# Kernel tuning notes

Measured on AMD Instinct MI355X. Metric: run time of the kernel, lower is better.

## Reference

```python
import jax, jax.numpy as jnp
import numpy as np

N_NODES = 100000


def sage_conv(x, src, dst, w_self, w_neigh, b):
    # DGL SAGEConv('mean'): h = x @ W_self + mean_{u in N(v)} x_u @ W_neigh + b
    ones = jnp.ones(src.shape[0], dtype=x.dtype)
    deg = jax.ops.segment_sum(ones, dst, num_segments=N_NODES)  # [N]
    neigh_sum = jax.ops.segment_sum(x[src], dst, num_segments=N_NODES)  # [N, F]
    neigh = neigh_sum / jnp.clip(deg, 1.0)[:, None]  # isolated nodes -> 0
    return x @ w_self + neigh @ w_neigh + b


def setup_inputs() -> dict:
    key = jax.random.key(0)
    ks = jax.random.split(key, 9)
    nfeat, nhid, nclass = 128, 128, 2
    E = 1600000
    x = jax.random.normal(ks[0], (N_NODES, nfeat), dtype=jnp.float32)
    src = jax.random.randint(ks[1], (E,), 0, N_NODES)
    dst = jax.random.randint(ks[2], (E,), 0, N_NODES)
    s1 = 1.0 / np.sqrt(nfeat)
    s2 = 1.0 / np.sqrt(nhid)
    return {
        "x": x,
        "src": src,
        "dst": dst,
        "w_self1": jax.random.uniform(ks[3], (nfeat, nhid), jnp.float32, -s1, s1),
        "w_neigh1": jax.random.uniform(ks[4], (nfeat, nhid), jnp.float32, -s1, s1),
        "b1": jnp.zeros((nhid,), jnp.float32),
        "w_self2": jax.random.uniform(ks[5], (nhid, nclass), jnp.float32, -s2, s2),
        "w_neigh2": jax.random.uniform(ks[6], (nhid, nclass), jnp.float32, -s2, s2),
        "b2": jnp.zeros((nclass,), jnp.float32),
    }


def reference(x, src, dst, w_self1, w_neigh1, b1, w_self2, w_neigh2, b2):
    h = jax.nn.relu(sage_conv(x, src, dst, w_self1, w_neigh1, b1))
    h = sage_conv(h, src, dst, w_self2, w_neigh2, b2)
    return jax.nn.log_softmax(h, axis=1)
```

## Files before the change

kernel.cpp:

```cpp
#include <hip/hip_runtime.h>
#include <hip/hip_bf16.h>


#define N_FEAT 128
#define CSHIFT 10
#define CNODES 1024
#define CCAP 18432
#define BATCH 4096
#define BF_BLOCKS 256
#define PW_BLOCKS 128

typedef __attribute__((ext_vector_type(8))) short short8;
typedef __attribute__((ext_vector_type(8))) unsigned short ushort8_t;
typedef __attribute__((ext_vector_type(16))) float f32x16;

__global__ __launch_bounds__(256) void prep_and_split_kernel(
    const int* __restrict__ src, const int* __restrict__ dst,
    int* __restrict__ ccursor, unsigned* __restrict__ cbuf, int E,
    const float* __restrict__ x, ushort* __restrict__ xb, int n4,
    const float* __restrict__ w1, const float* __restrict__ w2,
    ushort* __restrict__ wt, int nms) {
    __shared__ unsigned stage[BATCH];
    __shared__ int cntw[4][128];
    __shared__ int curw[4][128];
    __shared__ int s[128];
    __shared__ int excl[128];
    __shared__ int incl[128];
    __shared__ int gpos[128];
    int tid = threadIdx.x;
    int bid = blockIdx.x;

    if (bid >= nms) {
        int rb = bid - nms;
        if (rb < BF_BLOCKS) {
            int i = rb * 256 + tid;
            int stride = BF_BLOCKS * 256;
            for (; i < n4; i += stride) {
                float4 v = ((const float4*)x)[i];
                ushort4 r;
                r.x = __bfloat16_as_ushort(__float2bfloat16(v.x));
                r.y = __bfloat16_as_ushort(__float2bfloat16(v.y));
                r.z = __bfloat16_as_ushort(__float2bfloat16(v.z));
                r.w = __bfloat16_as_ushort(__float2bfloat16(v.w));
                ((ushort4*)xb)[i] = r;
            }
        } else {
            int id = (rb - BF_BLOCKS) * 256 + tid;
            int nn = id >> 8;
            int k = id & 255;
            float v = (k < 128) ? w1[k * 128 + nn] : w2[(k - 128) * 128 + nn];
            wt[nn * 256 + k] = __bfloat16_as_ushort(__float2bfloat16(v));
        }
        return;
    }

    int wv = tid >> 6;
    int base = bid * BATCH;
    int total = min(BATCH, E - base);

    unsigned pk[16];
    int bn[16];
    for (int i = tid; i < 512; i += 256) ((int*)cntw)[i] = 0;
    __syncthreads();
    #pragma unroll
    for (int k = 0; k < 16; ++k) {
        int e = base + k * 256 + tid;
        if (e < E) {
            int d = dst[e];
            int sv = src[e];
            bn[k] = d >> CSHIFT;
            pk[k] = ((unsigned)(d & (CNODES - 1)) << 17) | (unsigned)sv;
            atomicAdd(&cntw[wv][bn[k]], 1);
        } else {
            bn[k] = -1;
        }
    }
    __syncthreads();
    int c = 0;
    if (tid < 128) {
        int c0 = cntw[0][tid], c1 = cntw[1][tid], c2 = cntw[2][tid], c3 = cntw[3][tid];
        cntw[0][tid] = 0;
        cntw[1][tid] = c0;
        cntw[2][tid] = c0 + c1;
        cntw[3][tid] = c0 + c1 + c2;
        c = c0 + c1 + c2 + c3;
        s[tid] = c;
    }
    __syncthreads();
    int val = c;
    for (int off = 1; off < 128; off <<= 1) {
        int t = (tid >= off && tid < 128) ? s[tid - off] : 0;
        __syncthreads();
        if (tid < 128) { val += t; s[tid] = val; }
        __syncthreads();
    }
    if (tid < 128) {
        incl[tid] = val;
        int e0 = val - c;
        excl[tid] = e0;
        curw[0][tid] = e0 + cntw[0][tid];
        curw[1][tid] = e0 + cntw[1][tid];
        curw[2][tid] = e0 + cntw[2][tid];
        curw[3][tid] = e0 + cntw[3][tid];
        gpos[tid] = (c > 0) ? atomicAdd(&ccursor[tid], c) : 0;
    }
    __syncthreads();
    #pragma unroll
    for (int k = 0; k < 16; ++k) {
        if (bn[k] >= 0) {
            int ofs = atomicAdd(&curw[wv][bn[k]], 1);
            stage[ofs] = pk[k];
        }
    }
    __syncthreads();
    for (int i = tid; i < total; i += 256) {
        int lo = 0, hi = 127;
        while (lo < hi) {
            int mid = (lo + hi) >> 1;
            if (incl[mid] > i) hi = mid; else lo = mid + 1;
        }
        int b = lo;
        int target = gpos[b] + (i - excl[b]);
        cbuf[(size_t)b * CCAP + target] = stage[i];
    }
}

__global__ __launch_bounds__(1024) void build_csr2_kernel(
    const unsigned* __restrict__ cbuf, const int* __restrict__ ccnt,
    int* __restrict__ row_ptr, int* __restrict__ csr, int N, int E) {
    __shared__ int hist[CNODES];
    __shared__ int s[CNODES];
    __shared__ int cur[CNODES];
    __shared__ int cstart_s;
    int cb = blockIdx.x;
    int tid = threadIdx.x;

    int c0 = 0;
    if (tid < 128) { c0 = ccnt[tid]; s[tid] = c0; }
    __syncthreads();
    int v128 = c0;
    for (int off = 1; off < 128; off <<= 1) {
        int t = (tid >= off && tid < 128) ? s[tid - off] : 0;
        __syncthreads();
        if (tid < 128) { v128 += t; s[tid] = v128; }
        __syncthreads();
    }
    if (tid == cb) cstart_s = v128 - c0;
    if (cb == 0 && tid == 0) row_ptr[N] = E;
    __syncthreads();
    int cnt = ccnt[cb];
    int base = cstart_s;
    size_t bbase = (size_t)cb * CCAP;

    hist[tid] = 0;
    __syncthreads();
    for (int e = tid; e < cnt; e += 1024) {
        unsigned p = cbuf[bbase + e];
        atomicAdd(&hist[p >> 17], 1);
    }
    __syncthreads();
    int c = hist[tid];
    int val = c;
    s[tid] = val;
    __syncthreads();
    for (int off = 1; off < 1024; off <<= 1) {
        int t = (tid >= off) ? s[tid - off] : 0;
        __syncthreads();
        val += t;
        s[tid] = val;
        __syncthreads();
    }
    int excl = val - c;
    int node = cb * CNODES + tid;
    if (node < N) row_ptr[node] = base + excl;
    cur[tid] = excl;
    __syncthreads();
    for (int e = tid; e < cnt; e += 1024) {
        unsigned p = cbuf[bbase + e];
        int bin = p >> 17;
        int ofs = atomicAdd(&cur[bin], 1);
        csr[base + ofs] = (int)(p & 0x1FFFF);
    }
}

__device__ __forceinline__ float bf16_bits_to_f32(ushort u) {
    union { unsigned int i; float f; } c;
    c.i = ((unsigned int)u) << 16;
    return c.f;
}

__global__ void aggregate_bf16_kernel(const ushort* __restrict__ xb,
                                      const int* __restrict__ row_ptr,
                                      const int* __restrict__ csr,
                                      ushort* __restrict__ out, int n) {
    int v = blockIdx.x * 4 + (threadIdx.x >> 6);
    int lane = threadIdx.x & 63;
    if (v >= n) return;
    int beg = row_ptr[v];
    int end = row_ptr[v + 1];
    float a0 = 0.f, b0 = 0.f, a1 = 0.f, b1 = 0.f;
    int e = beg;
    for (; e + 8 <= end; e += 8) {
        int s0 = csr[e],     s1 = csr[e + 1], s2 = csr[e + 2], s3 = csr[e + 3];
        int s4 = csr[e + 4], s5 = csr[e + 5], s6 = csr[e + 6], s7 = csr[e + 7];
        ushort2 t0 = ((const ushort2*)(xb + (size_t)s0 * N_FEAT))[lane];
        ushort2 t1 = ((const ushort2*)(xb + (size_t)s1 * N_FEAT))[lane];
        ushort2 t2 = ((const ushort2*)(xb + (size_t)s2 * N_FEAT))[lane];
        ushort2 t3 = ((const ushort2*)(xb + (size_t)s3 * N_FEAT))[lane];
        ushort2 t4 = ((const ushort2*)(xb + (size_t)s4 * N_FEAT))[lane];
        ushort2 t5 = ((const ushort2*)(xb + (size_t)s5 * N_FEAT))[lane];
        ushort2 t6 = ((const ushort2*)(xb + (size_t)s6 * N_FEAT))[lane];
        ushort2 t7 = ((const ushort2*)(xb + (size_t)s7 * N_FEAT))[lane];
        a0 += bf16_bits_to_f32(t0.x); b0 += bf16_bits_to_f32(t0.y);
        a1 += bf16_bits_to_f32(t1.x); b1 += bf16_bits_to_f32(t1.y);
        a0 += bf16_bits_to_f32(t2.x); b0 += bf16_bits_to_f32(t2.y);
        a1 += bf16_bits_to_f32(t3.x); b1 += bf16_bits_to_f32(t3.y);
        a0 += bf16_bits_to_f32(t4.x); b0 += bf16_bits_to_f32(t4.y);
        a1 += bf16_bits_to_f32(t5.x); b1 += bf16_bits_to_f32(t5.y);
        a0 += bf16_bits_to_f32(t6.x); b0 += bf16_bits_to_f32(t6.y);
        a1 += bf16_bits_to_f32(t7.x); b1 += bf16_bits_to_f32(t7.y);
    }
    for (; e + 4 <= end; e += 4) {
        int s0 = csr[e], s1 = csr[e + 1], s2 = csr[e + 2], s3 = csr[e + 3];
        ushort2 t0 = ((const ushort2*)(xb + (size_t)s0 * N_FEAT))[lane];
        ushort2 t1 = ((const ushort2*)(xb + (size_t)s1 * N_FEAT))[lane];
        ushort2 t2 = ((const ushort2*)(xb + (size_t)s2 * N_FEAT))[lane];
        ushort2 t3 = ((const ushort2*)(xb + (size_t)s3 * N_FEAT))[lane];
        a0 += bf16_bits_to_f32(t0.x); b0 += bf16_bits_to_f32(t0.y);
        a1 += bf16_bits_to_f32(t1.x); b1 += bf16_bits_to_f32(t1.y);
        a0 += bf16_bits_to_f32(t2.x); b0 += bf16_bits_to_f32(t2.y);
        a1 += bf16_bits_to_f32(t3.x); b1 += bf16_bits_to_f32(t3.y);
    }
    for (; e < end; ++e) {
        int s0 = csr[e];
        ushort2 t0 = ((const ushort2*)(xb + (size_t)s0 * N_FEAT))[lane];
        a0 += bf16_bits_to_f32(t0.x); b0 += bf16_bits_to_f32(t0.y);
    }
    int deg = end - beg;
    float inv = (deg > 0) ? 1.0f / (float)deg : 0.0f;
    ushort2 r;
    r.x = __bfloat16_as_ushort(__float2bfloat16((a0 + a1) * inv));
    r.y = __bfloat16_as_ushort(__float2bfloat16((b0 + b1) * inv));
    ((ushort2*)(out + (size_t)v * N_FEAT))[lane] = r;
}

__global__ __launch_bounds__(256) void gemm1_fused_kernel(
    const ushort* __restrict__ xb, const ushort* __restrict__ nbb,
    const ushort* __restrict__ wt, const float* __restrict__ b,
    const float* __restrict__ ws2, const float* __restrict__ wn2,
    float* __restrict__ s_out, float* __restrict__ z_out, int n) {
    __shared__ ushort As[128 * 72];
    __shared__ ushort Bs[128 * 72];
    int tid = threadIdx.x;
    int wave = tid >> 6;
    int lane = tid & 63;
    int m = lane & 31;
    int half = lane >> 5;
    int block_row = blockIdx.x * 128;

    f32x16 acc[4];
    #pragma unroll
    for (int t = 0; t < 4; ++t)
        #pragma unroll
        for (int i = 0; i < 16; ++i) acc[t][i] = 0.0f;

    for (int kc = 0; kc < 4; ++kc) {
        const ushort* A = (kc < 2) ? xb : nbb;
        int k0 = (kc & 1) * 64;
        #pragma unroll
        for (int l = 0; l < 4; ++l) {
            int idx = l * 256 + tid;
            int r = idx >> 3;
            int p = idx & 7;
            int node = block_row + r;
            ushort8_t v;
            if (node < n) {
                v = *(const ushort8_t*)(A + (size_t)node * N_FEAT + k0 + p * 8);
            } else {
                #pragma unroll
                for (int q = 0; q < 8; ++q) v[q] = 0;
            }
            *(ushort8_t*)(&As[r * 72 + p * 8]) = v;
        }
        #pragma unroll
        for (int l = 0; l < 4; ++l) {
            int idx = l * 256 + tid;
            int cc = idx >> 3;
            int p = idx & 7;
            ushort8_t v = *(const ushort8_t*)(wt + (size_t)cc * 256 + kc * 64 + p * 8);
            *(ushort8_t*)(&Bs[cc * 72 + p * 8]) = v;
        }
        __syncthreads();
        #pragma unroll
        for (int ks = 0; ks < 4; ++ks) {
            int koff = ks * 16 + half * 8;
            short8 a = *(const short8*)(&As[(32 * wave + m) * 72 + koff]);
            short8 bf0 = *(const short8*)(&Bs[(0 * 32 + m) * 72 + koff]);
            short8 bf1 = *(const short8*)(&Bs[(1 * 32 + m) * 72 + koff]);
            short8 bf2 = *(const short8*)(&Bs[(2 * 32 + m) * 72 + koff]);
            short8 bf3 = *(const short8*)(&Bs[(3 * 32 + m) * 72 + koff]);
            acc[0] = __builtin_amdgcn_mfma_f32_32x32x16_bf16(a, bf0, acc[0], 0, 0, 0);
            acc[1] = __builtin_amdgcn_mfma_f32_32x32x16_bf16(a, bf1, acc[1], 0, 0, 0);
            acc[2] = __builtin_amdgcn_mfma_f32_32x32x16_bf16(a, bf2, acc[2], 0, 0, 0);
            acc[3] = __builtin_amdgcn_mfma_f32_32x32x16_bf16(a, bf3, acc[3], 0, 0, 0);
        }
        __syncthreads();
    }

    float bcol[4], wsc[4][2], wnc[4][2];
    #pragma unroll
    for (int t = 0; t < 4; ++t) {
        int col = t * 32 + m;
        bcol[t] = b[col];
        float2 a = ((const float2*)ws2)[col];
        float2 q = ((const float2*)wn2)[col];
        wsc[t][0] = a.x; wsc[t][1] = a.y;
        wnc[t][0] = q.x; wnc[t][1] = q.y;
    }
    #pragma unroll
    for (int reg = 0; reg < 16; ++reg) {
        int rowin = (reg & 3) + 8 * (reg >> 2) + 4 * half;
        int node = block_row + 32 * wave + rowin;
        float p0 = 0.f, p1 = 0.f, q0 = 0.f, q1 = 0.f;
        #pragma unroll
        for (int t = 0; t < 4; ++t) {
            float hv = fmaxf(acc[t][reg] + bcol[t], 0.0f);
            p0 += hv * wsc[t][0]; p1 += hv * wsc[t][1];
            q0 += hv * wnc[t][0]; q1 += hv * wnc[t][1];
        }
        #pragma unroll
        for (int off = 1; off < 32; off <<= 1) {
            p0 += __shfl_xor(p0, off);
            p1 += __shfl_xor(p1, off);
            q0 += __shfl_xor(q0, off);
            q1 += __shfl_xor(q1, off);
        }
        if (m == 0 && node < n) {
            ((float2*)s_out)[node] = make_float2(p0, p1);
            ((float2*)z_out)[node] = make_float2(q0, q1);
        }
    }
}

__global__ void layer2b_kernel(const float* __restrict__ s_in, const float* __restrict__ z,
                               const int* __restrict__ row_ptr, const int* __restrict__ csr,
                               const float* __restrict__ b, float* __restrict__ out, int n) {
    int v = blockIdx.x * 256 + threadIdx.x;
    if (v >= n) return;
    int beg = row_ptr[v];
    int end = row_ptr[v + 1];
    float a0 = 0.f, a1 = 0.f, c0 = 0.f, c1 = 0.f;
    int e = beg;
    for (; e + 2 <= end; e += 2) {
        float2 t0 = ((const float2*)z)[csr[e]];
        float2 t1 = ((const float2*)z)[csr[e + 1]];
        a0 += t0.x; a1 += t0.y;
        c0 += t1.x; c1 += t1.y;
    }
    if (e < end) {
        float2 t0 = ((const float2*)z)[csr[e]];
        a0 += t0.x; a1 += t0.y;
    }
    int deg = end - beg;
    float inv = (deg > 0) ? 1.0f / (float)deg : 0.0f;
    float2 sv = ((const float2*)s_in)[v];
    float o0 = sv.x + (a0 + c0) * inv + b[0];
    float o1 = sv.y + (a1 + c1) * inv + b[1];
    float mx = fmaxf(o0, o1);
    float lse = mx + logf(expf(o0 - mx) + expf(o1 - mx));
    ((float2*)out)[v] = make_float2(o0 - lse, o1 - lse);
}

extern "C" void kernel_launch(void* const* d_in, const int* in_sizes, int n_in,
                              void* d_out, int out_size, void* d_ws, size_t ws_size,
                              hipStream_t stream) {
    const float* x        = (const float*)d_in[0];
    const int*   src      = (const int*)d_in[1];
    const int*   dst      = (const int*)d_in[2];
    const float* w_self1  = (const float*)d_in[3];
    const float* w_neigh1 = (const float*)d_in[4];
    const float* b1       = (const float*)d_in[5];
    const float* w_self2  = (const float*)d_in[6];
    const float* w_neigh2 = (const float*)d_in[7];
    const float* b2       = (const float*)d_in[8];
    float* out = (float*)d_out;

    int N = in_sizes[0] / N_FEAT;
    int E = in_sizes[1];
    int nbk = (N + CNODES - 1) / CNODES;
    int nms = (E + BATCH - 1) / BATCH;

    char* ws = (char*)d_ws;
    size_t off = 0;
    auto alloc = [&](size_t bytes) -> void* {
        void* p = ws + off;
        off += (bytes + 255) & ~(size_t)255;
        return p;
    };
    int*      ccursor = (int*)alloc(128 * 4);
    int*      row_ptr = (int*)alloc((size_t)(N + 1) * 4);
    int*      csr     = (int*)alloc((size_t)E * 4);
    unsigned* cbuf    = (unsigned*)alloc((size_t)nbk * CCAP * 4);
    ushort*   xb      = (ushort*)alloc((size_t)N * N_FEAT * 2);
    ushort*   nbb     = (ushort*)alloc((size_t)N * N_FEAT * 2);
    ushort*   wt      = (ushort*)alloc((size_t)128 * 256 * 2);
    float*    s_buf   = (float*)alloc((size_t)N * 2 * 4);
    float*    z_buf   = (float*)alloc((size_t)N * 2 * 4);
    (void)ws_size; (void)n_in; (void)out_size;

    hipMemsetAsync(ccursor, 0, 128 * 4, stream);

    prep_and_split_kernel<<<nms + BF_BLOCKS + PW_BLOCKS, 256, 0, stream>>>(
        src, dst, ccursor, cbuf, E, x, xb, N * N_FEAT / 4, w_self1, w_neigh1, wt, nms);
    build_csr2_kernel<<<nbk, 1024, 0, stream>>>(cbuf, ccursor, row_ptr, csr, N, E);
    aggregate_bf16_kernel<<<(N + 3) / 4, 256, 0, stream>>>(xb, row_ptr, csr, nbb, N);
    gemm1_fused_kernel<<<(N + 127) / 128, 256, 0, stream>>>(
        xb, nbb, wt, b1, w_self2, w_neigh2, s_buf, z_buf, N);
    layer2b_kernel<<<(N + 255) / 256, 256, 0, stream>>>(s_buf, z_buf, row_ptr, csr, b2, out, N);
}
```

Before: 250.3 us.

## Use 16-byte gathers in aggregation and shuffle-based scans with 512-node CSR buckets

The aggregation kernel now splits each wave into four 16-lane groups. Each lane loads 8 bf16 features (16 bytes) per neighbor, so four neighbors are gathered in parallel, and the partial sums are combined with cross-lane shuffles. The bucket split moves to 256 bins of 512 nodes, which raises the number of CSR build blocks and lowers their size. The LDS-based prefix scans in both the split and build kernels become wave shuffle scans, cutting barrier counts. In exchange, the shuffle reductions add work and the bucket capacity per bin is tighter.

```diff
diff --git a/kernel.cpp b/kernel.cpp
--- a/kernel.cpp
+++ b/kernel.cpp
@@ -3,9 +3,10 @@
 
 
 #define N_FEAT 128
-#define CSHIFT 10
-#define CNODES 1024
-#define CCAP 18432
+#define CSHIFT 9
+#define CNODES 512
+#define NBINS 256
+#define CCAP 9728
 #define BATCH 4096
 #define BF_BLOCKS 256
 #define PW_BLOCKS 128
@@ -13,6 +14,12 @@
 typedef __attribute__((ext_vector_type(8))) short short8;
 typedef __attribute__((ext_vector_type(8))) unsigned short ushort8_t;
 typedef __attribute__((ext_vector_type(16))) float f32x16;
+
+__device__ __forceinline__ float bf16_bits_to_f32(ushort u) {
+    union { unsigned int i; float f; } c;
+    c.i = ((unsigned int)u) << 16;
+    return c.f;
+}
 
 __global__ __launch_bounds__(256) void prep_and_split_kernel(
     const int* __restrict__ src, const int* __restrict__ dst,
@@ -21,12 +28,12 @@
     const float* __restrict__ w1, const float* __restrict__ w2,
     ushort* __restrict__ wt, int nms) {
     __shared__ unsigned stage[BATCH];
-    __shared__ int cntw[4][128];
-    __shared__ int curw[4][128];
-    __shared__ int s[128];
-    __shared__ int excl[128];
-    __shared__ int incl[128];
-    __shared__ int gpos[128];
+    __shared__ int cntw[4][NBINS];
+    __shared__ int curw[4][NBINS];
+    __shared__ int excl[NBINS];
+    __shared__ int incl[NBINS];
+    __shared__ int gpos[NBINS];
+    __shared__ int wsum[4];
     int tid = threadIdx.x;
     int bid = blockIdx.x;
 
@@ -55,12 +62,13 @@
     }
 
     int wv = tid >> 6;
+    int lane = tid & 63;
     int base = bid * BATCH;
     int total = min(BATCH, E - base);
 
     unsigned pk[16];
     int bn[16];
-    for (int i = tid; i < 512; i += 256) ((int*)cntw)[i] = 0;
+    for (int i = tid; i < 4 * NBINS; i += 256) ((int*)cntw)[i] = 0;
     __syncthreads();
     #pragma unroll
     for (int k = 0; k < 16; ++k) {
@@ -76,34 +84,31 @@
         }
     }
     __syncthreads();
-    int c = 0;
-    if (tid < 128) {
-        int c0 = cntw[0][tid], c1 = cntw[1][tid], c2 = cntw[2][tid], c3 = cntw[3][tid];
-        cntw[0][tid] = 0;
-        cntw[1][tid] = c0;
-        cntw[2][tid] = c0 + c1;
-        cntw[3][tid] = c0 + c1 + c2;
-        c = c0 + c1 + c2 + c3;
-        s[tid] = c;
-    }
-    __syncthreads();
+    int c0 = cntw[0][tid], c1 = cntw[1][tid], c2 = cntw[2][tid], c3 = cntw[3][tid];
+    cntw[0][tid] = 0;
+    cntw[1][tid] = c0;
+    cntw[2][tid] = c0 + c1;
+    cntw[3][tid] = c0 + c1 + c2;
+    int c = c0 + c1 + c2 + c3;
     int val = c;
-    for (int off = 1; off < 128; off <<= 1) {
-        int t = (tid >= off && tid < 128) ? s[tid - off] : 0;
-        __syncthreads();
-        if (tid < 128) { val += t; s[tid] = val; }
-        __syncthreads();
-    }
-    if (tid < 128) {
-        incl[tid] = val;
-        int e0 = val - c;
-        excl[tid] = e0;
-        curw[0][tid] = e0 + cntw[0][tid];
-        curw[1][tid] = e0 + cntw[1][tid];
-        curw[2][tid] = e0 + cntw[2][tid];
-        curw[3][tid] = e0 + cntw[3][tid];
-        gpos[tid] = (c > 0) ? atomicAdd(&ccursor[tid], c) : 0;
-    }
+    #pragma unroll
+    for (int off = 1; off < 64; off <<= 1) {
+        int t = __shfl_up(val, off);
+        if (lane >= off) val += t;
+    }
+    if (lane == 63) wsum[wv] = val;
+    __syncthreads();
+    #pragma unroll
+    for (int i = 0; i < 4; ++i)
+        if (i < wv) val += wsum[i];
+    incl[tid] = val;
+    int e0 = val - c;
+    excl[tid] = e0;
+    curw[0][tid] = e0 + cntw[0][tid];
+    curw[1][tid] = e0 + cntw[1][tid];
+    curw[2][tid] = e0 + cntw[2][tid];
+    curw[3][tid] = e0 + cntw[3][tid];
+    gpos[tid] = (c > 0) ? atomicAdd(&ccursor[tid], c) : 0;
     __syncthreads();
     #pragma unroll
     for (int k = 0; k < 16; ++k) {
@@ -114,7 +119,7 @@
     }
     __syncthreads();
     for (int i = tid; i < total; i += 256) {
-        int lo = 0, hi = 127;
+        int lo = 0, hi = NBINS - 1;
         while (lo < hi) {
             int mid = (lo + hi) >> 1;
             if (incl[mid] > i) hi = mid; else lo = mid + 1;
@@ -125,57 +130,59 @@
     }
 }
 
-__global__ __launch_bounds__(1024) void build_csr2_kernel(
+__global__ __launch_bounds__(512) void build_csr2_kernel(
     const unsigned* __restrict__ cbuf, const int* __restrict__ ccnt,
     int* __restrict__ row_ptr, int* __restrict__ csr, int N, int E) {
     __shared__ int hist[CNODES];
-    __shared__ int s[CNODES];
     __shared__ int cur[CNODES];
+    __shared__ int wred[8];
     __shared__ int cstart_s;
     int cb = blockIdx.x;
     int tid = threadIdx.x;
-
-    int c0 = 0;
-    if (tid < 128) { c0 = ccnt[tid]; s[tid] = c0; }
-    __syncthreads();
-    int v128 = c0;
-    for (int off = 1; off < 128; off <<= 1) {
-        int t = (tid >= off && tid < 128) ? s[tid - off] : 0;
-        __syncthreads();
-        if (tid < 128) { v128 += t; s[tid] = v128; }
-        __syncthreads();
-    }
-    if (tid == cb) cstart_s = v128 - c0;
+    int lane = tid & 63;
+    int w = tid >> 6;
+
+    int v = (tid < cb) ? ccnt[tid] : 0;
+    #pragma unroll
+    for (int off = 32; off > 0; off >>= 1) v += __shfl_xor(v, off);
+    if (lane == 0) wred[w] = v;
+    hist[tid] = 0;
+    __syncthreads();
+    if (tid == 0) {
+        int t = 0;
+        #pragma unroll
+        for (int i = 0; i < 8; ++i) t += wred[i];
+        cstart_s = t;
+    }
     if (cb == 0 && tid == 0) row_ptr[N] = E;
-    __syncthreads();
     int cnt = ccnt[cb];
+    size_t bbase = (size_t)cb * CCAP;
+    __syncthreads();
     int base = cstart_s;
-    size_t bbase = (size_t)cb * CCAP;
-
-    hist[tid] = 0;
-    __syncthreads();
-    for (int e = tid; e < cnt; e += 1024) {
+
+    for (int e = tid; e < cnt; e += 512) {
         unsigned p = cbuf[bbase + e];
         atomicAdd(&hist[p >> 17], 1);
     }
     __syncthreads();
     int c = hist[tid];
     int val = c;
-    s[tid] = val;
-    __syncthreads();
-    for (int off = 1; off < 1024; off <<= 1) {
-        int t = (tid >= off) ? s[tid - off] : 0;
-        __syncthreads();
-        val += t;
-        s[tid] = val;
-        __syncthreads();
-    }
+    #pragma unroll
+    for (int off = 1; off < 64; off <<= 1) {
+        int t = __shfl_up(val, off);
+        if (lane >= off) val += t;
+    }
+    if (lane == 63) wred[w] = val;
+    __syncthreads();
+    #pragma unroll
+    for (int i = 0; i < 8; ++i)
+        if (i < w) val += wred[i];
     int excl = val - c;
     int node = cb * CNODES + tid;
     if (node < N) row_ptr[node] = base + excl;
     cur[tid] = excl;
     __syncthreads();
-    for (int e = tid; e < cnt; e += 1024) {
+    for (int e = tid; e < cnt; e += 512) {
         unsigned p = cbuf[bbase + e];
         int bin = p >> 17;
         int ofs = atomicAdd(&cur[bin], 1);
@@ -183,65 +190,78 @@
     }
 }
 
-__device__ __forceinline__ float bf16_bits_to_f32(ushort u) {
-    union { unsigned int i; float f; } c;
-    c.i = ((unsigned int)u) << 16;
-    return c.f;
-}
-
-__global__ void aggregate_bf16_kernel(const ushort* __restrict__ xb,
-                                      const int* __restrict__ row_ptr,
-                                      const int* __restrict__ csr,
-                                      ushort* __restrict__ out, int n) {
+__global__ __launch_bounds__(256) void aggregate_bf16_kernel(
+    const ushort* __restrict__ xb, const int* __restrict__ row_ptr,
+    const int* __restrict__ csr, ushort* __restrict__ out, int n) {
     int v = blockIdx.x * 4 + (threadIdx.x >> 6);
     int lane = threadIdx.x & 63;
+    int sub = lane >> 4;
+    int fc = lane & 15;
     if (v >= n) return;
     int beg = row_ptr[v];
     int end = row_ptr[v + 1];
-    float a0 = 0.f, b0 = 0.f, a1 = 0.f, b1 = 0.f;
+    float acc[8];
+    #pragma unroll
+    for (int j = 0; j < 8; ++j) acc[j] = 0.f;
+    const ushort* xfc = xb + fc * 8;
     int e = beg;
-    for (; e + 8 <= end; e += 8) {
-        int s0 = csr[e],     s1 = csr[e + 1], s2 = csr[e + 2], s3 = csr[e + 3];
-        int s4 = csr[e + 4], s5 = csr[e + 5], s6 = csr[e + 6], s7 = csr[e + 7];
-        ushort2 t0 = ((const ushort2*)(xb + (size_t)s0 * N_FEAT))[lane];
-        ushort2 t1 = ((const ushort2*)(xb + (size_t)s1 * N_FEAT))[lane];
-        ushort2 t2 = ((const ushort2*)(xb + (size_t)s2 * N_FEAT))[lane];
-        ushort2 t3 = ((const ushort2*)(xb + (size_t)s3 * N_FEAT))[lane];
-        ushort2 t4 = ((const ushort2*)(xb + (size_t)s4 * N_FEAT))[lane];
-        ushort2 t5 = ((const ushort2*)(xb + (size_t)s5 * N_FEAT))[lane];
-        ushort2 t6 = ((const ushort2*)(xb + (size_t)s6 * N_FEAT))[lane];
-        ushort2 t7 = ((const ushort2*)(xb + (size_t)s7 * N_FEAT))[lane];
-        a0 += bf16_bits_to_f32(t0.x); b0 += bf16_bits_to_f32(t0.y);
-        a1 += bf16_bits_to_f32(t1.x); b1 += bf16_bits_to_f32(t1.y);
-        a0 += bf16_bits_to_f32(t2.x); b0 += bf16_bits_to_f32(t2.y);
-        a1 += bf16_bits_to_f32(t3.x); b1 += bf16_bits_to_f32(t3.y);
-        a0 += bf16_bits_to_f32(t4.x); b0 += bf16_bits_to_f32(t4.y);
-        a1 += bf16_bits_to_f32(t5.x); b1 += bf16_bits_to_f32(t5.y);
-        a0 += bf16_bits_to_f32(t6.x); b0 += bf16_bits_to_f32(t6.y);
-        a1 += bf16_bits_to_f32(t7.x); b1 += bf16_bits_to_f32(t7.y);
-    }
-    for (; e + 4 <= end; e += 4) {
-        int s0 = csr[e], s1 = csr[e + 1], s2 = csr[e + 2], s3 = csr[e + 3];
-        ushort2 t0 = ((const ushort2*)(xb + (size_t)s0 * N_FEAT))[lane];
-        ushort2 t1 = ((const ushort2*)(xb + (size_t)s1 * N_FEAT))[lane];
-        ushort2 t2 = ((const ushort2*)(xb + (size_t)s2 * N_FEAT))[lane];
-        ushort2 t3 = ((const ushort2*)(xb + (size_t)s3 * N_FEAT))[lane];
-        a0 += bf16_bits_to_f32(t0.x); b0 += bf16_bits_to_f32(t0.y);
-        a1 += bf16_bits_to_f32(t1.x); b1 += bf16_bits_to_f32(t1.y);
-        a0 += bf16_bits_to_f32(t2.x); b0 += bf16_bits_to_f32(t2.y);
-        a1 += bf16_bits_to_f32(t3.x); b1 += bf16_bits_to_f32(t3.y);
-    }
-    for (; e < end; ++e) {
-        int s0 = csr[e];
-        ushort2 t0 = ((const ushort2*)(xb + (size_t)s0 * N_FEAT))[lane];
-        a0 += bf16_bits_to_f32(t0.x); b0 += bf16_bits_to_f32(t0.y);
-    }
-    int deg = end - beg;
-    float inv = (deg > 0) ? 1.0f / (float)deg : 0.0f;
-    ushort2 r;
-    r.x = __bfloat16_as_ushort(__float2bfloat16((a0 + a1) * inv));
-    r.y = __bfloat16_as_ushort(__float2bfloat16((b0 + b1) * inv));
-    ((ushort2*)(out + (size_t)v * N_FEAT))[lane] = r;
+    for (; e + 16 <= end; e += 16) {
+        int s0 = csr[e + sub];
+        int s1 = csr[e + 4 + sub];
+        int s2 = csr[e + 8 + sub];
+        int s3 = csr[e + 12 + sub];
+        ushort8_t t0 = *(const ushort8_t*)(xfc + (size_t)s0 * N_FEAT);
+        ushort8_t t1 = *(const ushort8_t*)(xfc + (size_t)s1 * N_FEAT);
+        ushort8_t t2 = *(const ushort8_t*)(xfc + (size_t)s2 * N_FEAT);
+        ushort8_t t3 = *(const ushort8_t*)(xfc + (size_t)s3 * N_FEAT);
+        #pragma unroll
+        for (int j = 0; j < 8; ++j) acc[j] += bf16_bits_to_f32(t0[j]);
+        #pragma unroll
+        for (int j = 0; j < 8; ++j) acc[j] += bf16_bits_to_f32(t1[j]);
+        #pragma unroll
+        for (int j = 0; j < 8; ++j) acc[j] += bf16_bits_to_f32(t2[j]);
+        #pragma unroll
+        for (int j = 0; j < 8; ++j) acc[j] += bf16_bits_to_f32(t3[j]);
+    }
+    if (e + 8 <= end) {
+        int s0 = csr[e + sub];
+        int s1 = csr[e + 4 + sub];
+        ushort8_t t0 = *(const ushort8_t*)(xfc + (size_t)s0 * N_FEAT);
+        ushort8_t t1 = *(const ushort8_t*)(xfc + (size_t)s1 * N_FEAT);
+        #pragma unroll
+        for (int j = 0; j < 8; ++j) acc[j] += bf16_bits_to_f32(t0[j]);
+        #pragma unroll
+        for (int j = 0; j < 8; ++j) acc[j] += bf16_bits_to_f32(t1[j]);
+        e += 8;
+    }
+    if (e + 4 <= end) {
+        int s0 = csr[e + sub];
+        ushort8_t t0 = *(const ushort8_t*)(xfc + (size_t)s0 * N_FEAT);
+        #pragma unroll
+        for (int j = 0; j < 8; ++j) acc[j] += bf16_bits_to_f32(t0[j]);
+        e += 4;
+    }
+    int rem = end - e;
+    if (sub < rem) {
+        int s0 = csr[e + sub];
+        ushort8_t t0 = *(const ushort8_t*)(xfc + (size_t)s0 * N_FEAT);
+        #pragma unroll
+        for (int j = 0; j < 8; ++j) acc[j] += bf16_bits_to_f32(t0[j]);
+    }
+    #pragma unroll
+    for (int j = 0; j < 8; ++j) {
+        acc[j] += __shfl_xor(acc[j], 16);
+        acc[j] += __shfl_xor(acc[j], 32);
+    }
+    if (lane < 16) {
+        int deg = end - beg;
+        float inv = (deg > 0) ? 1.0f / (float)deg : 0.0f;
+        ushort8_t r;
+        #pragma unroll
+        for (int j = 0; j < 8; ++j)
+            r[j] = __bfloat16_as_ushort(__float2bfloat16(acc[j] * inv));
+        *(ushort8_t*)(out + (size_t)v * N_FEAT + lane * 8) = r;
+    }
 }
 
 __global__ __launch_bounds__(256) void gemm1_fused_kernel(
@@ -397,7 +417,7 @@
         off += (bytes + 255) & ~(size_t)255;
         return p;
     };
-    int*      ccursor = (int*)alloc(128 * 4);
+    int*      ccursor = (int*)alloc(NBINS * 4);
     int*      row_ptr = (int*)alloc((size_t)(N + 1) * 4);
     int*      csr     = (int*)alloc((size_t)E * 4);
     unsigned* cbuf    = (unsigned*)alloc((size_t)nbk * CCAP * 4);
@@ -408,11 +428,11 @@
     float*    z_buf   = (float*)alloc((size_t)N * 2 * 4);
     (void)ws_size; (void)n_in; (void)out_size;
 
-    hipMemsetAsync(ccursor, 0, 128 * 4, stream);
+    hipMemsetAsync(ccursor, 0, NBINS * 4, stream);
 
     prep_and_split_kernel<<<nms + BF_BLOCKS + PW_BLOCKS, 256, 0, stream>>>(
         src, dst, ccursor, cbuf, E, x, xb, N * N_FEAT / 4, w_self1, w_neigh1, wt, nms);
-    build_csr2_kernel<<<nbk, 1024, 0, stream>>>(cbuf, ccursor, row_ptr, csr, N, E);
+    build_csr2_kernel<<<nbk, 512, 0, stream>>>(cbuf, ccursor, row_ptr, csr, N, E);
     aggregate_bf16_kernel<<<(N + 3) / 4, 256, 0, stream>>>(xb, row_ptr, csr, nbb, N);
     gemm1_fused_kernel<<<(N + 127) / 128, 256, 0, stream>>>(
         xb, nbb, wt, b1, w_self2, w_neigh2, s_buf, z_buf, N);
```

After: 244.6 us. 1.02x faster.
